# Kernel optimization log

Measured on AMD Instinct MI355X. Metric: run time of the kernel, lower is better.

Reference implementation:

```python
import jax, jax.numpy as jnp
import numpy as np

N_HEAD = 16
HEAD_DIM = 64


def setup_inputs() -> dict:
    key = jax.random.key(0)
    k1, k2, k3 = jax.random.split(key, 3)
    B, T, C = 1, 4096, 1024
    x = jax.random.normal(k1, (B, T, C), dtype=jnp.float32)
    w_attn = jax.random.normal(k2, (3 * C, C), dtype=jnp.float32) * (C ** -0.5)
    w_proj = jax.random.normal(k3, (C, C), dtype=jnp.float32) * (C ** -0.5)
    return {"x": x, "w_attn": w_attn, "w_proj": w_proj}


def reference(x, w_attn, w_proj):
    B, T, C = x.shape
    H, D = N_HEAD, HEAD_DIM
    qkv = jnp.einsum('btc,fc->btf', x, w_attn)  # [B,T,3C]
    q, k, v = jnp.split(qkv, 3, axis=-1)
    # [B,H,T,D]
    q = q.reshape(B, T, H, D).transpose(0, 2, 1, 3)
    k = k.reshape(B, T, H, D).transpose(0, 2, 1, 3)
    v = v.reshape(B, T, H, D).transpose(0, 2, 1, 3)
    scale = 1.0 / (D ** 0.5)
    att = jnp.einsum('bhqd,bhkd->bhqk', q, k) * scale  # [B,H,T,T]
    causal = jnp.tril(jnp.ones((T, T), dtype=bool))
    att = jnp.where(causal[None, None], att, -jnp.inf)
    att = jax.nn.softmax(att, axis=-1)
    y = jnp.einsum('bhqk,bhkd->bhqd', att, v)  # [B,H,T,D]
    y = y.transpose(0, 2, 1, 3).reshape(B, T, C)
    return jnp.einsum('btc,oc->bto', y, w_proj)
```

## Files before the change

### kernel.cpp

```cpp
#include <hip/hip_runtime.h>

typedef unsigned short u16;
typedef __bf16 bf16x8 __attribute__((ext_vector_type(8)));
typedef float f32x4 __attribute__((ext_vector_type(4)));

__device__ __forceinline__ u16 f2bf(float f) {
  union { float f; unsigned u; } v; v.f = f;
  return (u16)((v.u + 0x7fffu + ((v.u >> 16) & 1u)) >> 16);
}

__device__ __forceinline__ unsigned pkbf(float lo, float hi) {
  union { float f; unsigned u; } a, b; a.f = lo; b.f = hi;
  return __builtin_amdgcn_perm(b.u + 0x8000u, a.u + 0x8000u, 0x07060302u);
}

__device__ __forceinline__ float fexp2(float x) {
#if __has_builtin(__builtin_amdgcn_exp2f)
  return __builtin_amdgcn_exp2f(x);
#else
  return exp2f(x);
#endif
}

__device__ __forceinline__ void gld16(const u16* g, u16* l) {
  __builtin_amdgcn_global_load_lds(
      (const __attribute__((address_space(1))) void*)g,
      (__attribute__((address_space(3))) void*)l, 16, 0, 0);
}


__global__ __launch_bounds__(256) void cvt3(
    const float* __restrict__ x, const float* __restrict__ wa,
    const float* __restrict__ wp, u16* __restrict__ xb,
    u16* __restrict__ wab, u16* __restrict__ wpb)
{
  int b = blockIdx.x;
  const float* in; u16* out; int i;
  if (b < 2048)      { in = x;  out = xb;  i = b * 256 + threadIdx.x; }
  else if (b < 3584) { in = wa; out = wab; i = (b - 2048) * 256 + threadIdx.x; }
  else               { in = wp; out = wpb; i = (b - 3584) * 256 + threadIdx.x; }
  const float* p = in + (size_t)i * 8;
  float4 a = *(const float4*)p, c = *(const float4*)(p + 4);
  uint4 o;
  o.x = pkbf(a.x, a.y); o.y = pkbf(a.z, a.w);
  o.z = pkbf(c.x, c.y); o.w = pkbf(c.z, c.w);
  *(uint4*)&out[(size_t)i * 8] = o;
}

template<bool COUT_F32, bool VSPLIT>
__global__ __launch_bounds__(256, 3) void gemm_lds(
    const u16* __restrict__ A, const u16* __restrict__ B, void* __restrict__ C,
    u16* __restrict__ C2, int M, int N, int K, int ldc)
{
  __shared__ u16 S[9216];
  u16* As = S;
  u16* Bs = S + 4096;
  const int tid  = threadIdx.x;
  const int wave = tid >> 6, lane = tid & 63;
  const int quad = lane >> 4, ln = lane & 15;
  const int m0 = blockIdx.y * 128, n0 = blockIdx.x * 128;
  const int wm = (wave >> 1) * 64, wn = (wave & 1) * 64;

  const int srow = wave * 32 + (lane >> 2);
  const int scol = (lane & 3) * 8;

  f32x4 acc[4][4] = {};

  for (int k0 = 0; k0 < K; k0 += 32) {
    __syncthreads();
    const u16* ga = A + (size_t)(m0 + srow) * K + k0 + scol;
    const u16* gb = B + (size_t)(n0 + srow) * K + k0 + scol;
    gld16(ga,                  As + wave * 1024);
    gld16(ga + (size_t)16 * K, As + wave * 1024 + 512);
    gld16(gb,                  Bs + wave * 1024);
    gld16(gb + (size_t)16 * K, Bs + wave * 1024 + 512);
    __syncthreads();

    bf16x8 af[4], bfr[4];
#pragma unroll
    for (int i = 0; i < 4; ++i) af[i]  = *(const bf16x8*)&As[(wm + i * 16 + ln) * 32 + quad * 8];
#pragma unroll
    for (int j = 0; j < 4; ++j) bfr[j] = *(const bf16x8*)&Bs[(wn + j * 16 + ln) * 32 + quad * 8];
#pragma unroll
    for (int i = 0; i < 4; ++i)
#pragma unroll
      for (int j = 0; j < 4; ++j)
        acc[i][j] = __builtin_amdgcn_mfma_f32_16x16x32_bf16(af[i], bfr[j], acc[i][j], 0, 0, 0);
  }

  if constexpr (VSPLIT) {
    if (n0 >= 2048) {
      u16 (*Cs)[72] = (u16(*)[72])S;
      __syncthreads();
#pragma unroll
      for (int c = 0; c < 2; ++c) {
        if ((wave >> 1) == c) {
#pragma unroll
          for (int i = 0; i < 4; ++i)
#pragma unroll
            for (int j = 0; j < 4; ++j)
#pragma unroll
              for (int r = 0; r < 4; ++r) {
                int pos = (i >> 1) * 32 + quad * 8 + (i & 1) * 4 + r;
                Cs[wn + j * 16 + ln][pos] = f2bf(acc[i][j][r]);
              }
        }
        __syncthreads();
        {
          int nl = tid >> 1, mseg = (tid & 1) * 32;
#pragma unroll
          for (int s2 = 0; s2 < 4; ++s2) {
            uint4 v4 = *(const uint4*)&Cs[nl][mseg + s2 * 8];
            *(uint4*)&C2[(size_t)(n0 - 2048 + nl) * 4096 + m0 + c * 64 + mseg + s2 * 8] = v4;
          }
        }
        __syncthreads();
      }
      return;
    }
  }

#pragma unroll
  for (int i = 0; i < 4; ++i)
#pragma unroll
    for (int j = 0; j < 4; ++j)
#pragma unroll
      for (int r = 0; r < 4; ++r) {
        int m = m0 + wm + i * 16 + quad * 4 + r;
        int n = n0 + wn + j * 16 + ln;
        if constexpr (COUT_F32)
          ((float*)C)[(size_t)m * ldc + n] = acc[i][j][r];
        else
          ((u16*)C)[(size_t)m * ldc + n] = f2bf(acc[i][j][r]);
      }
}

template<bool COUT_F32>
__global__ __launch_bounds__(256, 4) void gemm_t64(
    const u16* __restrict__ A, const u16* __restrict__ B, void* __restrict__ C,
    int M, int N, int K, int ldc)
{
  __shared__ u16 S[4096];
  u16* As = S;
  u16* Bs = S + 2048;
  const int tid  = threadIdx.x;
  const int wave = tid >> 6, lane = tid & 63;
  const int quad = lane >> 4, ln = lane & 15;
  const int m0 = blockIdx.y * 64, n0 = blockIdx.x * 64;

  const int srow = wave * 16 + (lane >> 2);
  const int scol = (lane & 3) * 8;

  f32x4 acc[4] = {};

  for (int k0 = 0; k0 < K; k0 += 32) {
    __syncthreads();
    gld16(A + (size_t)(m0 + srow) * K + k0 + scol, As + wave * 512);
    gld16(B + (size_t)(n0 + srow) * K + k0 + scol, Bs + wave * 512);
    __syncthreads();

    bf16x8 af = *(const bf16x8*)&As[(wave * 16 + ln) * 32 + quad * 8];
#pragma unroll
    for (int j = 0; j < 4; ++j) {
      bf16x8 bf = *(const bf16x8*)&Bs[(j * 16 + ln) * 32 + quad * 8];
      acc[j] = __builtin_amdgcn_mfma_f32_16x16x32_bf16(af, bf, acc[j], 0, 0, 0);
    }
  }

#pragma unroll
  for (int j = 0; j < 4; ++j)
#pragma unroll
    for (int r = 0; r < 4; ++r) {
      int m = m0 + wave * 16 + quad * 4 + r;
      int n = n0 + j * 16 + ln;
      if constexpr (COUT_F32)
        ((float*)C)[(size_t)m * ldc + n] = acc[j][r];
      else
        ((u16*)C)[(size_t)m * ldc + n] = f2bf(acc[j][r]);
    }
}

template<bool F32>
__device__ __forceinline__ void stage8(u16* dst, const void* base, size_t off) {
  if constexpr (F32) {
    const float* p = (const float*)base + off;
    float4 a = *(const float4*)p;
    float4 b = *(const float4*)(p + 4);
    uint4 q;
    q.x = pkbf(a.x, a.y); q.y = pkbf(a.z, a.w);
    q.z = pkbf(b.x, b.y); q.w = pkbf(b.z, b.w);
    *(uint4*)dst = q;
  } else {
    *(uint4*)dst = *(const uint4*)((const u16*)base + off);
  }
}

template<bool AF32, bool BF32, bool COUT_F32, bool VSPLIT>
__global__ __launch_bounds__(256) void gemm_bt(
    const void* __restrict__ A, const void* __restrict__ B, void* __restrict__ C,
    u16* __restrict__ C2, int M, int N, int K, int ldc)
{
  __shared__ u16 As[128][40];
  __shared__ u16 Bs[128][40];
  const int tid  = threadIdx.x;
  const int wave = tid >> 6, lane = tid & 63;
  const int quad = lane >> 4, ln = lane & 15;
  const int m0 = blockIdx.y * 128, n0 = blockIdx.x * 128;
  const int wm = (wave >> 1) * 64, wn = (wave & 1) * 64;

  f32x4 acc[4][4] = {};

  for (int k0 = 0; k0 < K; k0 += 32) {
    __syncthreads();
#pragma unroll
    for (int i = 0; i < 2; ++i) {
      int idx = tid + i * 256;
      int row = idx >> 2, seg = (idx & 3) * 8;
      stage8<AF32>(&As[row][seg], A, (size_t)(m0 + row) * K + k0 + seg);
      stage8<BF32>(&Bs[row][seg], B, (size_t)(n0 + row) * K + k0 + seg);
    }
    __syncthreads();
    bf16x8 af[4], bfr[4];
#pragma unroll
    for (int i = 0; i < 4; ++i) af[i]  = *(const bf16x8*)&As[wm + i * 16 + ln][quad * 8];
#pragma unroll
    for (int j = 0; j < 4; ++j) bfr[j] = *(const bf16x8*)&Bs[wn + j * 16 + ln][quad * 8];
#pragma unroll
    for (int i = 0; i < 4; ++i)
#pragma unroll
      for (int j = 0; j < 4; ++j)
        acc[i][j] = __builtin_amdgcn_mfma_f32_16x16x32_bf16(af[i], bfr[j], acc[i][j], 0, 0, 0);
  }

  if constexpr (VSPLIT) {
    if (n0 >= 2048) {
      __shared__ u16 Cs[128][72];
#pragma unroll
      for (int c = 0; c < 2; ++c) {
        if ((wave >> 1) == c) {
#pragma unroll
          for (int i = 0; i < 4; ++i)
#pragma unroll
            for (int j = 0; j < 4; ++j)
#pragma unroll
              for (int r = 0; r < 4; ++r) {
                int pos = (i >> 1) * 32 + quad * 8 + (i & 1) * 4 + r;
                Cs[wn + j * 16 + ln][pos] = f2bf(acc[i][j][r]);
              }
        }
        __syncthreads();
        {
          int nl = tid >> 1, mseg = (tid & 1) * 32;
#pragma unroll
          for (int s2 = 0; s2 < 4; ++s2) {
            uint4 v4 = *(const uint4*)&Cs[nl][mseg + s2 * 8];
            *(uint4*)&C2[(size_t)(n0 - 2048 + nl) * 4096 + m0 + c * 64 + mseg + s2 * 8] = v4;
          }
        }
        __syncthreads();
      }
      return;
    }
  }

#pragma unroll
  for (int i = 0; i < 4; ++i)
#pragma unroll
    for (int j = 0; j < 4; ++j)
#pragma unroll
      for (int r = 0; r < 4; ++r) {
        int m = m0 + wm + i * 16 + quad * 4 + r;
        int n = n0 + wn + j * 16 + ln;
        if constexpr (COUT_F32)
          ((float*)C)[(size_t)m * ldc + n] = acc[i][j][r];
        else
          ((u16*)C)[(size_t)m * ldc + n] = f2bf(acc[i][j][r]);
      }
}

struct StageRegs { uint4 k0, k1, v0, v1; };

__device__ __forceinline__ StageRegs attn_stage_load(
    const u16* __restrict__ qk, const u16* __restrict__ vT,
    int h, int kbase, int tid) {
  StageRegs s;
  {
    int key = tid >> 2, seg = (tid & 3) * 16;
    const u16* kp = qk + (size_t)(kbase + key) * 2048 + 1024 + h * 64 + seg;
    s.k0 = *(const uint4*)kp;
    s.k1 = *(const uint4*)(kp + 8);
  }
  {
    int kh = tid >> 7, d = (tid >> 1) & 63, sg = (tid & 1) * 16;
    const u16* vp = vT + (size_t)(h * 64 + d) * 4096 + kbase + kh * 32 + sg;
    s.v0 = *(const uint4*)vp;
    s.v1 = *(const uint4*)(vp + 8);
  }
  return s;
}

__global__ __launch_bounds__(256, 2) void attn_fwd(
    const u16* __restrict__ qk, const u16* __restrict__ vT, u16* __restrict__ y)
{
  __shared__ u16 Ks[2][2][64][40];
  __shared__ u16 Vt[2][2][64][40];

  const int tid  = threadIdx.x;
  const int wave = tid >> 6, lane = tid & 63;
  const int quad = lane >> 4, ln = lane & 15;
  const int bx = blockIdx.x;
  const int qt = (bx < 256) ? (31 - (bx >> 4)) : ((bx - 256) >> 4);
  const int h  = bx & 15;
  const float C1 = 0.18033688f;

  const int sq0[2] = { qt * 128 + wave * 32, qt * 128 + wave * 32 + 16 };

  bf16x8 qa[2][2];
#pragma unroll
  for (int s = 0; s < 2; ++s) {
    const u16* qrow = qk + (size_t)(sq0[s] + ln) * 2048 + h * 64;
    qa[s][0] = *(const bf16x8*)(qrow + quad * 8);
    qa[s][1] = *(const bf16x8*)(qrow + 32 + quad * 8);
  }

  f32x4 o[2][4] = {};
  float l_i[2] = {0.f, 0.f};

  StageRegs st = attn_stage_load(qk, vT, h, 0, tid);
  const int ktmax = 2 * qt + 1;
  int b = 0;
  for (int kt = 0; kt <= ktmax; ++kt, b ^= 1) {
    {
      int key = tid >> 2, seg = (tid & 3) * 16;
      int kh = seg >> 5, off = seg & 31;
      *(uint4*)&Ks[b][kh][key][off]     = st.k0;
      *(uint4*)&Ks[b][kh][key][off + 8] = st.k1;
      int vh = tid >> 7, d = (tid >> 1) & 63, sg = (tid & 1) * 16;
      *(uint4*)&Vt[b][vh][d][sg]     = st.v0;
      *(uint4*)&Vt[b][vh][d][sg + 8] = st.v1;
    }
    __syncthreads();
    if (kt < ktmax) st = attn_stage_load(qk, vT, h, (kt + 1) * 64, tid);

    bf16x8 kf[2][4], vb[2][4];
#pragma unroll
    for (int hf = 0; hf < 2; ++hf)
#pragma unroll
      for (int c = 0; c < 4; ++c) {
        kf[hf][c] = *(const bf16x8*)&Ks[b][hf][c * 16 + ln][quad * 8];
        vb[hf][c] = *(const bf16x8*)&Vt[b][hf][c * 16 + ln][quad * 8];
      }

    bool act[2];
#pragma unroll
    for (int s = 0; s < 2; ++s) act[s] = (kt * 64 <= sq0[s] + 15);

    bf16x8 pb[2][2];
#pragma unroll
    for (int s = 0; s < 2; ++s) {
      if (!act[s]) continue;
      f32x4 sv[4];
#pragma unroll
      for (int t = 0; t < 4; ++t) {
        f32x4 z = {0.f, 0.f, 0.f, 0.f};
        z = __builtin_amdgcn_mfma_f32_16x16x32_bf16(kf[0][t], qa[s][0], z, 0, 0, 0);
        z = __builtin_amdgcn_mfma_f32_16x16x32_bf16(kf[1][t], qa[s][1], z, 0, 0, 0);
        sv[t] = z;
      }
      float p[4][4];
      if (kt * 64 + 63 > sq0[s]) {
        const int qr = sq0[s] + ln;
#pragma unroll
        for (int t = 0; t < 4; ++t) {
          int keyb = kt * 64 + t * 16 + quad * 4;
#pragma unroll
          for (int r = 0; r < 4; ++r) {
            float arg = (keyb + r > qr) ? -200.0f : fmaf(sv[t][r], C1, -46.0f);
            p[t][r] = fexp2(arg);
          }
        }
      } else {
#pragma unroll
        for (int t = 0; t < 4; ++t)
#pragma unroll
          for (int r = 0; r < 4; ++r)
            p[t][r] = fexp2(fmaf(sv[t][r], C1, -46.0f));
      }
#pragma unroll
      for (int t = 0; t < 4; ++t)
        l_i[s] += (p[t][0] + p[t][1]) + (p[t][2] + p[t][3]);
#pragma unroll
      for (int H = 0; H < 2; ++H) {
        union { unsigned u[4]; bf16x8 v; } pk;
        pk.u[0] = pkbf(p[2 * H][0],     p[2 * H][1]);
        pk.u[1] = pkbf(p[2 * H][2],     p[2 * H][3]);
        pk.u[2] = pkbf(p[2 * H + 1][0], p[2 * H + 1][1]);
        pk.u[3] = pkbf(p[2 * H + 1][2], p[2 * H + 1][3]);
        pb[s][H] = pk.v;
      }
    }

#pragma unroll
    for (int s = 0; s < 2; ++s) {
      if (!act[s]) continue;
#pragma unroll
      for (int dt = 0; dt < 4; ++dt) {
        f32x4 z = o[s][dt];
        z = __builtin_amdgcn_mfma_f32_16x16x32_bf16(vb[0][dt], pb[s][0], z, 0, 0, 0);
        z = __builtin_amdgcn_mfma_f32_16x16x32_bf16(vb[1][dt], pb[s][1], z, 0, 0, 0);
        o[s][dt] = z;
      }
    }
  }

#pragma unroll
  for (int s = 0; s < 2; ++s) {
    l_i[s] += __shfl_xor(l_i[s], 16);
    l_i[s] += __shfl_xor(l_i[s], 32);
    float inv = 1.0f / l_i[s];
    int rowg = sq0[s] + ln;
#pragma unroll
    for (int dt = 0; dt < 4; ++dt)
#pragma unroll
      for (int r = 0; r < 4; ++r)
        y[(size_t)rowg * 1024 + h * 64 + dt * 16 + quad * 4 + r] = f2bf(o[s][dt][r] * inv);
  }
}

extern "C" void kernel_launch(void* const* d_in, const int* in_sizes, int n_in,
                              void* d_out, int out_size, void* d_ws, size_t ws_size,
                              hipStream_t stream) {
  const float* x      = (const float*)d_in[0];
  const float* w_attn = (const float*)d_in[1];
  const float* w_proj = (const float*)d_in[2];

  char* ws = (char*)d_ws;
  u16* qk = (u16*)ws;
  u16* vT = (u16*)(ws + (16u << 20));

  if (ws_size >= (size_t)(40u << 20)) {
    u16* wpb = (u16*)(ws + (24u << 20));
    u16* xb  = (u16*)(ws + (26u << 20));
    u16* wab = (u16*)(ws + (34u << 20));
    u16* y   = (u16*)(ws + (26u << 20));

    cvt3<<<4096, 256, 0, stream>>>(x, w_attn, w_proj, xb, wab, wpb);
    gemm_lds<false, true><<<dim3(24, 32), 256, 0, stream>>>(
        xb, wab, qk, vT, 4096, 3072, 1024, 2048);
    attn_fwd<<<dim3(512), 256, 0, stream>>>(qk, vT, y);
    gemm_t64<true><<<dim3(16, 64), 256, 0, stream>>>(
        y, wpb, d_out, 4096, 1024, 1024, 1024);
  } else {
    u16* y = (u16*)(ws + (24u << 20));
    gemm_bt<true, true, false, true><<<dim3(24, 32), 256, 0, stream>>>(
        x, w_attn, qk, vT, 4096, 3072, 1024, 2048);
    attn_fwd<<<dim3(512), 256, 0, stream>>>(qk, vT, y);
    gemm_bt<false, true, true, false><<<dim3(8, 32), 256, 0, stream>>>(
        y, w_proj, d_out, nullptr, 4096, 1024, 1024, 1024);
  }
}
```

Before: 204.9 us.

## Split causal attention key range across two blocks and merge partials

Each query tile's key loop is split into two halves handled by separate blocks, doubling the attention grid to 1024 blocks and raising the occupancy hint to 4. Each half writes unnormalized bf16 partial outputs and row sums, and a new combine kernel adds the two halves and normalizes. This targets load imbalance and under-filled CUs in the causal attention kernel. The cost is an extra kernel launch, roughly 24 MB of extra partial-output traffic, and an extra bf16 rounding of the unnormalized partials.

```diff
diff --git a/kernel.cpp b/kernel.cpp
--- a/kernel.cpp
+++ b/kernel.cpp
@@ -7,6 +7,10 @@
 __device__ __forceinline__ u16 f2bf(float f) {
   union { float f; unsigned u; } v; v.f = f;
   return (u16)((v.u + 0x7fffu + ((v.u >> 16) & 1u)) >> 16);
+}
+__device__ __forceinline__ float bf2f(u16 h) {
+  union { unsigned u; float f; } v; v.u = ((unsigned)h) << 16;
+  return v.f;
 }
 
 __device__ __forceinline__ unsigned pkbf(float lo, float hi) {
@@ -47,6 +51,30 @@
   *(uint4*)&out[(size_t)i * 8] = o;
 }
 
+__global__ __launch_bounds__(256) void combine2(
+    const u16* __restrict__ O0, const u16* __restrict__ O1,
+    const float* __restrict__ l0, const float* __restrict__ l1,
+    u16* __restrict__ y)
+{
+  int i = blockIdx.x * 256 + threadIdx.x;
+  int e0 = i * 8;
+  int row = e0 >> 10, h = (e0 & 1023) >> 6;
+  float inv = 1.0f / (l0[row * 16 + h] + l1[row * 16 + h]);
+  uint4 a = *(const uint4*)&O0[(size_t)e0];
+  uint4 b = *(const uint4*)&O1[(size_t)e0];
+  unsigned aw[4] = {a.x, a.y, a.z, a.w}, bw[4] = {b.x, b.y, b.z, b.w};
+  uint4 o;
+  unsigned ow[4];
+#pragma unroll
+  for (int j = 0; j < 4; ++j) {
+    float lo = (bf2f((u16)(aw[j] & 0xffffu)) + bf2f((u16)(bw[j] & 0xffffu))) * inv;
+    float hi = (bf2f((u16)(aw[j] >> 16))     + bf2f((u16)(bw[j] >> 16)))     * inv;
+    ow[j] = pkbf(lo, hi);
+  }
+  o.x = ow[0]; o.y = ow[1]; o.z = ow[2]; o.w = ow[3];
+  *(uint4*)&y[(size_t)e0] = o;
+}
+
 template<bool COUT_F32, bool VSPLIT>
 __global__ __launch_bounds__(256, 3) void gemm_lds(
     const u16* __restrict__ A, const u16* __restrict__ B, void* __restrict__ C,
@@ -299,8 +327,11 @@
   return s;
 }
 
-__global__ __launch_bounds__(256, 2) void attn_fwd(
-    const u16* __restrict__ qk, const u16* __restrict__ vT, u16* __restrict__ y)
+template<bool SPLIT>
+__global__ __launch_bounds__(256, SPLIT ? 4 : 2) void attn_fwd(
+    const u16* __restrict__ qk, const u16* __restrict__ vT,
+    u16* __restrict__ out0, u16* __restrict__ out1,
+    float* __restrict__ l0buf, float* __restrict__ l1buf)
 {
   __shared__ u16 Ks[2][2][64][40];
   __shared__ u16 Vt[2][2][64][40];
@@ -309,8 +340,22 @@
   const int wave = tid >> 6, lane = tid & 63;
   const int quad = lane >> 4, ln = lane & 15;
   const int bx = blockIdx.x;
-  const int qt = (bx < 256) ? (31 - (bx >> 4)) : ((bx - 256) >> 4);
-  const int h  = bx & 15;
+  int qt, h, ktb, kte;
+  u16* oout; float* lout;
+  if constexpr (SPLIT) {
+    qt = 31 - (bx >> 5);
+    int half = (bx >> 4) & 1;
+    h = bx & 15;
+    ktb = half ? (qt + 1) : 0;
+    kte = half ? (2 * qt + 1) : qt;
+    oout = half ? out1 : out0;
+    lout = half ? l1buf : l0buf;
+  } else {
+    qt = (bx < 256) ? (31 - (bx >> 4)) : ((bx - 256) >> 4);
+    h = bx & 15;
+    ktb = 0; kte = 2 * qt + 1;
+    oout = out0; lout = nullptr;
+  }
   const float C1 = 0.18033688f;
 
   const int sq0[2] = { qt * 128 + wave * 32, qt * 128 + wave * 32 + 16 };
@@ -326,10 +371,9 @@
   f32x4 o[2][4] = {};
   float l_i[2] = {0.f, 0.f};
 
-  StageRegs st = attn_stage_load(qk, vT, h, 0, tid);
-  const int ktmax = 2 * qt + 1;
+  StageRegs st = attn_stage_load(qk, vT, h, ktb * 64, tid);
   int b = 0;
-  for (int kt = 0; kt <= ktmax; ++kt, b ^= 1) {
+  for (int kt = ktb; kt <= kte; ++kt, b ^= 1) {
     {
       int key = tid >> 2, seg = (tid & 3) * 16;
       int kh = seg >> 5, off = seg & 31;
@@ -340,7 +384,7 @@
       *(uint4*)&Vt[b][vh][d][sg + 8] = st.v1;
     }
     __syncthreads();
-    if (kt < ktmax) st = attn_stage_load(qk, vT, h, (kt + 1) * 64, tid);
+    if (kt < kte) st = attn_stage_load(qk, vT, h, (kt + 1) * 64, tid);
 
     bf16x8 kf[2][4], vb[2][4];
 #pragma unroll
@@ -417,13 +461,22 @@
   for (int s = 0; s < 2; ++s) {
     l_i[s] += __shfl_xor(l_i[s], 16);
     l_i[s] += __shfl_xor(l_i[s], 32);
-    float inv = 1.0f / l_i[s];
     int rowg = sq0[s] + ln;
-#pragma unroll
-    for (int dt = 0; dt < 4; ++dt)
-#pragma unroll
-      for (int r = 0; r < 4; ++r)
-        y[(size_t)rowg * 1024 + h * 64 + dt * 16 + quad * 4 + r] = f2bf(o[s][dt][r] * inv);
+    if constexpr (SPLIT) {
+#pragma unroll
+      for (int dt = 0; dt < 4; ++dt)
+#pragma unroll
+        for (int r = 0; r < 4; ++r)
+          oout[(size_t)rowg * 1024 + h * 64 + dt * 16 + quad * 4 + r] = f2bf(o[s][dt][r]);
+      if (quad == 0) lout[rowg * 16 + h] = l_i[s];
+    } else {
+      float inv = 1.0f / l_i[s];
+#pragma unroll
+      for (int dt = 0; dt < 4; ++dt)
+#pragma unroll
+        for (int r = 0; r < 4; ++r)
+          oout[(size_t)rowg * 1024 + h * 64 + dt * 16 + quad * 4 + r] = f2bf(o[s][dt][r] * inv);
+    }
   }
 }
 
@@ -438,7 +491,24 @@
   u16* qk = (u16*)ws;
   u16* vT = (u16*)(ws + (16u << 20));
 
-  if (ws_size >= (size_t)(40u << 20)) {
+  if (ws_size >= (size_t)(44u << 20)) {
+    u16*   wpb = (u16*)(ws + (24u << 20));
+    u16*   xb  = (u16*)(ws + (26u << 20));
+    u16*   wab = (u16*)(ws + (34u << 20));
+    u16*   Op0 = (u16*)(ws + (26u << 20));
+    u16*   Op1 = (u16*)(ws + (34u << 20));
+    float* l0  = (float*)(ws + (42u << 20));
+    float* l1  = (float*)(ws + (42u << 20) + (256u << 10));
+    u16*   y   = (u16*)ws;
+
+    cvt3<<<4096, 256, 0, stream>>>(x, w_attn, w_proj, xb, wab, wpb);
+    gemm_lds<false, true><<<dim3(24, 32), 256, 0, stream>>>(
+        xb, wab, qk, vT, 4096, 3072, 1024, 2048);
+    attn_fwd<true><<<dim3(1024), 256, 0, stream>>>(qk, vT, Op0, Op1, l0, l1);
+    combine2<<<2048, 256, 0, stream>>>(Op0, Op1, l0, l1, y);
+    gemm_t64<true><<<dim3(16, 64), 256, 0, stream>>>(
+        y, wpb, d_out, 4096, 1024, 1024, 1024);
+  } else if (ws_size >= (size_t)(40u << 20)) {
     u16* wpb = (u16*)(ws + (24u << 20));
     u16* xb  = (u16*)(ws + (26u << 20));
     u16* wab = (u16*)(ws + (34u << 20));
@@ -447,14 +517,14 @@
     cvt3<<<4096, 256, 0, stream>>>(x, w_attn, w_proj, xb, wab, wpb);
     gemm_lds<false, true><<<dim3(24, 32), 256, 0, stream>>>(
         xb, wab, qk, vT, 4096, 3072, 1024, 2048);
-    attn_fwd<<<dim3(512), 256, 0, stream>>>(qk, vT, y);
+    attn_fwd<false><<<dim3(512), 256, 0, stream>>>(qk, vT, y, nullptr, nullptr, nullptr);
     gemm_t64<true><<<dim3(16, 64), 256, 0, stream>>>(
         y, wpb, d_out, 4096, 1024, 1024, 1024);
   } else {
     u16* y = (u16*)(ws + (24u << 20));
     gemm_bt<true, true, false, true><<<dim3(24, 32), 256, 0, stream>>>(
         x, w_attn, qk, vT, 4096, 3072, 1024, 2048);
-    attn_fwd<<<dim3(512), 256, 0, stream>>>(qk, vT, y);
+    attn_fwd<false><<<dim3(512), 256, 0, stream>>>(qk, vT, y, nullptr, nullptr, nullptr);
     gemm_bt<false, true, true, false><<<dim3(8, 32), 256, 0, stream>>>(
         y, w_proj, d_out, nullptr, 4096, 1024, 1024, 1024);
   }
```

New measurement: 457.6 us. +123.3%, slower.
